# Performance work log

Measured on AMD Instinct MI355X. Metric: run time of the kernel, lower is better.

The kernel has to match this reference:

```python
import jax, jax.numpy as jnp
import numpy as np

B, H, W, DIM = 1, 320, 320, 256
WIN, NH = 10, 8
HD = DIM // NH
N = WIN * WIN
HID = 4 * DIM
SCALE = HD ** (-0.5)
EPS = 1e-5


def _rel_pos_index():
    coords = np.stack(np.meshgrid(np.arange(WIN), np.arange(WIN), indexing='ij'))  # [2,w,w]
    cf = coords.reshape(2, -1)                      # [2, N]
    rel = (cf[:, :, None] - cf[:, None, :]).transpose(1, 2, 0).astype(np.int64)  # [N,N,2]
    rel[:, :, 0] += WIN - 1
    rel[:, :, 1] += WIN - 1
    rel[:, :, 0] *= 2 * WIN - 1
    return jnp.asarray(rel.sum(-1))                 # [N, N]

REL_IDX = _rel_pos_index()


def setup_inputs() -> dict:
    key = jax.random.key(0)
    ks = jax.random.split(key, 16)
    std = 0.02
    return {
        'x': jax.random.normal(ks[0], (B, H * W, DIM), jnp.float32),
        'norm1_g': jnp.ones((DIM,), jnp.float32),
        'norm1_b': jnp.zeros((DIM,), jnp.float32),
        'wq': jax.random.normal(ks[1], (DIM, DIM), jnp.float32) * std,
        'bq': jnp.zeros((DIM,), jnp.float32),
        'wkv': jax.random.normal(ks[2], (DIM, 2 * DIM), jnp.float32) * std,
        'bkv': jnp.zeros((2 * DIM,), jnp.float32),
        'rpb': jax.random.normal(ks[3], ((2 * WIN - 1) ** 2, NH), jnp.float32) * std,
        'proj_w': jax.random.normal(ks[4], (DIM, DIM), jnp.float32) * std,
        'proj_b': jnp.zeros((DIM,), jnp.float32),
        'norm2_g': jnp.ones((DIM,), jnp.float32),
        'norm2_b': jnp.zeros((DIM,), jnp.float32),
        'l1_w': jax.random.normal(ks[5], (DIM, HID), jnp.float32) * std,
        'l1_b': jnp.zeros((HID,), jnp.float32),
        'dw_w': jax.random.normal(ks[6], (HID, 1, 3, 3), jnp.float32) * std,
        'dw_b': jnp.zeros((HID,), jnp.float32),
        'l2_w': jax.random.normal(ks[7], (HID, DIM), jnp.float32) * std,
        'l2_b': jnp.zeros((DIM,), jnp.float32),
    }


def _ln(x, g, b):
    m = x.mean(-1, keepdims=True)
    v = ((x - m) ** 2).mean(-1, keepdims=True)
    return (x - m) * jax.lax.rsqrt(v + EPS) * g + b


def reference(x, norm1_g, norm1_b, wq, bq, wkv, bkv, rpb, proj_w, proj_b,
              norm2_g, norm2_b, l1_w, l1_b, dw_w, dw_b, l2_w, l2_b):
    # ---- Window attention branch ----
    h = _ln(x, norm1_g, norm1_b).reshape(B, H, W, DIM)
    # window partition: [B*nW, N, C]
    win = h.reshape(B, H // WIN, WIN, W // WIN, WIN, DIM)
    win = win.transpose(0, 1, 3, 2, 4, 5).reshape(-1, N, DIM)
    q = (win @ wq + bq).reshape(-1, N, NH, HD).transpose(0, 2, 1, 3) * SCALE  # [bW,h,N,d]
    kv = (win @ wkv + bkv).reshape(-1, N, 2, NH, HD).transpose(2, 0, 3, 1, 4)
    k, v = kv[0], kv[1]                                                        # [bW,h,N,d]
    attn = jnp.einsum('bhnd,bhmd->bhnm', q, k)                                 # [bW,h,N,N]
    bias = rpb[REL_IDX]                                                        # [N,N,h]
    attn = attn + bias.transpose(2, 0, 1)[None]
    attn = jax.nn.softmax(attn, axis=-1)
    o = jnp.einsum('bhnm,bhmd->bhnd', attn, v).transpose(0, 2, 1, 3).reshape(-1, N, DIM)
    o = o @ proj_w + proj_b
    # window reverse: [B, H*W, C]
    o = o.reshape(B, H // WIN, W // WIN, WIN, WIN, DIM)
    o = o.transpose(0, 1, 3, 2, 4, 5).reshape(B, H * W, DIM)
    x = x + o
    # ---- LeFF branch ----
    h2 = _ln(x, norm2_g, norm2_b)
    f = jax.nn.gelu(h2 @ l1_w + l1_b, approximate=False)
    f = f.reshape(B, H, W, HID).transpose(0, 3, 1, 2)                          # NCHW
    f = jax.lax.conv_general_dilated(
        f, dw_w, window_strides=(1, 1), padding='SAME',
        feature_group_count=HID,
        dimension_numbers=('NCHW', 'OIHW', 'NCHW')) + dw_b[None, :, None, None]
    f = jax.nn.gelu(f, approximate=False)
    f = f.transpose(0, 2, 3, 1).reshape(B, H * W, HID)
    x = x + (f @ l2_w + l2_b)
    return x
```

## Files before the change

kernel.cpp:

```cpp
#include <hip/hip_runtime.h>
#include <hip/hip_bf16.h>

typedef unsigned short u16;
typedef __attribute__((ext_vector_type(8))) __bf16 bf16x8;
typedef __attribute__((ext_vector_type(4))) float f32x4;

#define HW_ 320
#define DIM_ 256
#define HID_ 1024
#define SCALE_ 0.1767766952966369f
#define LDP 72
#define NEGINF_ -30000.0f

__device__ __forceinline__ float b2f(u16 u){
  union{unsigned int i; float f;} z; z.i=((unsigned int)u)<<16; return z.f;
}
__device__ __forceinline__ u16 f2b(float f){
  union{float f; unsigned int i;} z; z.f=f;
  return (u16)((z.i + 0x7fffu + ((z.i>>16)&1u))>>16);
}
__device__ __forceinline__ u16 f2b_s(float f, float sub){
  union{float f; unsigned int i;} z; z.f=f;
  if ((z.i & 0x7F800000u) == 0x7F800000u) z.f = sub;
  return (u16)((z.i + 0x7fffu + ((z.i>>16)&1u))>>16);
}
__device__ __forceinline__ float gelu_f(float v){
  float u = 0.7978845608028654f*(v + 0.044715f*v*v*v);
  float e = __expf(2.f*u);
  float t = 1.f - 2.f/(e+1.f);
  return 0.5f*v*(1.f+t);
}

__global__ void k_transpose(const float* __restrict__ src, u16* __restrict__ dst, int K, int N){
  int i = blockIdx.x*256 + threadIdx.x;
  if (i < K*N){ int k = i / N, n = i - k*N; dst[(size_t)n*K + k] = f2b(src[i]); }
}
__global__ void k_transpose_dw(const float* __restrict__ src, u16* __restrict__ dst){
  int i = blockIdx.x*256 + threadIdx.x;
  if (i < 9216){ int ch = i / 9, kk = i - ch*9; dst[kk*1024 + ch] = f2b(src[i]); }
}
__global__ void k_qkvbias(const float* __restrict__ bq, const float* __restrict__ bkv, float* __restrict__ dst){
  int i = blockIdx.x*256 + threadIdx.x;
  if (i < 768) dst[i] = (i<256) ? bq[i] : bkv[i-256];
}
__global__ void k_biastab(const float* __restrict__ rpb, float* __restrict__ btab){
  int i = blockIdx.x*256 + threadIdx.x;
  if (i >= 114688) return;
  int ct = i & 7, lr = (i>>3) & 15;
  int idx = i >> 7;
  int n = idx % 112, h = idx / 112;
  int m = ct*16 + lr;
  float v = NEGINF_;
  if (n < 100 && m < 100){
    int rel = (n/10 - m/10 + 9)*19 + (n%10 - m%10 + 9);
    v = rpb[rel*8 + h];
  }
  btab[i] = v;
}

template<int F32IN, int WINDOWED>
__global__ __launch_bounds__(256) void k_ln(const void* __restrict__ xv,
    const float* __restrict__ g, const float* __restrict__ b, u16* __restrict__ out)
{
  int tid = threadIdx.x, lane = tid & 63;
  int t = blockIdx.x*4 + (tid>>6);
  float v[4];
  if constexpr (F32IN){
    float4 f = *(const float4*)((const float*)xv + (size_t)t*DIM_ + lane*4);
    v[0]=f.x; v[1]=f.y; v[2]=f.z; v[3]=f.w;
  } else {
    uint2 u = *(const uint2*)((const u16*)xv + (size_t)t*DIM_ + lane*4);
    v[0]=b2f((u16)(u.x&0xffff)); v[1]=b2f((u16)(u.x>>16));
    v[2]=b2f((u16)(u.y&0xffff)); v[3]=b2f((u16)(u.y>>16));
  }
  float s  = v[0]+v[1]+v[2]+v[3];
  float ss = v[0]*v[0]+v[1]*v[1]+v[2]*v[2]+v[3]*v[3];
  for (int m=1;m<64;m<<=1){ s += __shfl_xor(s,m,64); ss += __shfl_xor(ss,m,64); }
  float mean = s*(1.0f/DIM_);
  float var  = ss*(1.0f/DIM_) - mean*mean;
  if (var < 0.f) var = 0.f;
  float rstd = rsqrtf(var + 1e-5f);
  float4 gg = *(const float4*)(g + lane*4);
  float4 bb = *(const float4*)(b + lane*4);
  float o0 = (v[0]-mean)*rstd*gg.x + bb.x;
  float o1 = (v[1]-mean)*rstd*gg.y + bb.y;
  float o2 = (v[2]-mean)*rstd*gg.z + bb.z;
  float o3 = (v[3]-mean)*rstd*gg.w + bb.w;
  int row = t;
  if constexpr (WINDOWED){
    int hy = t / HW_, wx = t - hy*HW_;
    row = ((hy/10)*32 + wx/10)*100 + (hy%10)*10 + (wx%10);
  }
  unsigned lo = (unsigned)f2b(o0) | ((unsigned)f2b(o1)<<16);
  unsigned hi = (unsigned)f2b(o2) | ((unsigned)f2b(o3)<<16);
  *(uint2*)(out + (size_t)row*DIM_ + lane*4) = make_uint2(lo,hi);
}

template<int EPI, int CLAMP>
__global__ __launch_bounds__(512,2) void k_gemm(
    const u16* __restrict__ A, const u16* __restrict__ Bt, int K, int nx,
    const float* __restrict__ biasf,
    const float* __restrict__ resf, const u16* __restrict__ resb,
    u16* __restrict__ O0, u16* __restrict__ O1, u16* __restrict__ O2,
    float* __restrict__ Of,
    int a_off, int o_off, int mguard)
{
  __shared__ u16 Al[256*LDP];
  __shared__ u16 Bl[128*LDP];
  int tid = threadIdx.x;
  int bid = blockIdx.x, nwg = gridDim.x;
  int swz = (bid & 7)*(nwg>>3) + (bid>>3);
  int m0 = (swz / nx)*256, n0 = (swz % nx)*128;
  int w = tid>>6, lane = tid&63, lr = lane&15, lg = lane>>4;
  int wrow = (w>>1)*64, wcol = (w&1)*64;
  f32x4 zero = {0.f,0.f,0.f,0.f};
  f32x4 acc[4][4];
  #pragma unroll
  for (int i=0;i<4;++i)
    #pragma unroll
    for (int j=0;j<4;++j) acc[i][j]=zero;

  for (int kt=0; kt<K; kt+=64){
    #pragma unroll
    for (int it=0; it<4; ++it){
      int vi = tid + it*512;
      int row = vi>>3, cv = (vi&7)*8;
      int srow = m0 + row;
      if constexpr (CLAMP){
        srow += a_off;
        srow = srow < 0 ? 0 : (srow > 102399 ? 102399 : srow);
      }
      *(bf16x8*)&Al[row*LDP+cv] = *(const bf16x8*)(A + (size_t)srow*K + kt + cv);
    }
    #pragma unroll
    for (int it=0; it<2; ++it){
      int vi = tid + it*512;
      int row = vi>>3, cv = (vi&7)*8;
      *(bf16x8*)&Bl[row*LDP+cv] = *(const bf16x8*)(Bt + (size_t)(n0+row)*K + kt + cv);
    }
    __syncthreads();
    #pragma unroll
    for (int k0=0;k0<64;k0+=32){
      bf16x8 af[4], bfr[4];
      #pragma unroll
      for (int i=0;i<4;++i) af[i]  = *(const bf16x8*)&Al[(wrow+i*16+lr)*LDP + k0 + lg*8];
      #pragma unroll
      for (int j=0;j<4;++j) bfr[j] = *(const bf16x8*)&Bl[(wcol+j*16+lr)*LDP + k0 + lg*8];
      #pragma unroll
      for (int i=0;i<4;++i)
        #pragma unroll
        for (int j=0;j<4;++j)
          acc[i][j] = __builtin_amdgcn_mfma_f32_16x16x32_bf16(af[i], bfr[j], acc[i][j],0,0,0);
    }
    __syncthreads();
  }

  float bj[4];
  #pragma unroll
  for (int j=0;j<4;++j) bj[j] = biasf[n0 + wcol + j*16 + lr];

  #pragma unroll
  for (int i=0;i<4;++i){
    #pragma unroll
    for (int r=0;r<4;++r){
      int grow = m0 + wrow + i*16 + lg*4 + r;
      if constexpr (EPI==0){
        int winl = grow/100, n = grow - winl*100;
        size_t rowb = ((size_t)winl*8)*3200 + (size_t)n*32;
        #pragma unroll
        for (int j=0;j<4;++j){
          int gcol = n0 + wcol + j*16 + lr;
          float v = acc[i][j][r] + bj[j];
          int part = gcol>>8, c = gcol&255;
          size_t idx = rowb + (size_t)(c>>5)*3200 + (c&31);
          if (part==0)      O0[idx] = f2b_s(v*SCALE_, 10000.f);
          else if (part==1) O1[idx] = f2b_s(v, 10000.f);
          else              O2[idx] = f2b_s(v, 10000.f);
        }
      } else if constexpr (EPI==1){
        int win = grow/100, n = grow - win*100;
        int wy = win>>5, wxx = win&31;
        int py = n/10, px = n - py*10;
        size_t t = (size_t)((wy*10+py)*HW_ + wxx*10 + px);
        #pragma unroll
        for (int j=0;j<4;++j){
          int gcol = n0 + wcol + j*16 + lr;
          float o = acc[i][j][r] + bj[j] + resf[t*DIM_ + gcol];
          O0[t*DIM_ + gcol] = f2b_s(o, 30000.f);
        }
      } else if constexpr (EPI==2){
        if (grow < mguard){
          #pragma unroll
          for (int j=0;j<4;++j){
            int gcol = n0 + wcol + j*16 + lr;
            float o = gelu_f(acc[i][j][r] + bj[j]);
            O0[(size_t)grow*HID_ + gcol] = f2b_s(o, 40000.f);
          }
        }
      } else {
        size_t t = (size_t)(o_off + grow);
        #pragma unroll
        for (int j=0;j<4;++j){
          int gcol = n0 + wcol + j*16 + lr;
          float o = acc[i][j][r] + bj[j] + b2f(resb[t*DIM_ + gcol]);
          union{float f; unsigned int i;} z; z.f=o;
          if ((z.i & 0x7F800000u) == 0x7F800000u) o = 60000.f;
          Of[t*DIM_ + gcol] = o;
        }
      }
    }
  }
}

__global__ __launch_bounds__(256) void k_attn(
    const u16* __restrict__ Q, const u16* __restrict__ Kb, const u16* __restrict__ Vb,
    const float* __restrict__ btab, u16* __restrict__ Ow)
{
  __shared__ u16 p_lds[112*136];
  __shared__ u16 v_t[32*136];
  int tid = threadIdx.x;
  int wh = blockIdx.x;
  int head = wh & 7, win = wh >> 3;
  for (int i=tid;i<896;i+=256){ int row=i>>3, c=i&7; *(unsigned*)&p_lds[row*136 + 112 + 2*c] = 0u; }
  for (int i=tid;i<576;i+=256){ int d=i/18, c=i-18*d; *(unsigned*)&v_t[d*136 + 100 + 2*c] = 0u; }
  __syncthreads();
  const u16* vbase = Vb + (size_t)wh*3200;
  for (int i=tid;i<1600;i+=256){
    int m=i>>4, d2=(i&15)<<1;
    unsigned u = *(const unsigned*)(vbase + m*32 + d2);
    v_t[d2*136+m]     = (u16)(u&0xffff);
    v_t[(d2+1)*136+m] = (u16)(u>>16);
  }

  int w = tid>>6, lane = tid&63, lr = lane&15, lg = lane>>4;
  const u16* qbase = Q  + (size_t)wh*3200;
  const u16* kbase = Kb + (size_t)wh*3200;
  f32x4 zero = {0.f,0.f,0.f,0.f};
  bf16x8 aq[2];
  #pragma unroll
  for (int rt=0;rt<2;++rt){
    int qr = w*32 + rt*16 + lr; if (qr>99) qr=99;
    aq[rt] = *(const bf16x8*)(qbase + qr*32 + lg*8);
  }
  f32x4 s[2][7];
  #pragma unroll
  for (int ct=0;ct<7;++ct){
    int kr = ct*16 + lr; if (kr>99) kr=99;
    bf16x8 bk = *(const bf16x8*)(kbase + kr*32 + lg*8);
    s[0][ct] = __builtin_amdgcn_mfma_f32_16x16x32_bf16(aq[0], bk, zero,0,0,0);
    s[1][ct] = __builtin_amdgcn_mfma_f32_16x16x32_bf16(aq[1], bk, zero,0,0,0);
  }
  float inv[2][4];
  #pragma unroll
  for (int rt=0;rt<2;++rt){
    #pragma unroll
    for (int r=0;r<4;++r){
      int n = w*32 + rt*16 + lg*4 + r;
      int nb = n < 112 ? n : 111;
      const float* brow = btab + (((size_t)(head*112 + nb))*16 + lr)*8;
      float4 b0 = *(const float4*)brow;
      float4 b1 = *(const float4*)(brow + 4);
      float bias7[7] = {b0.x,b0.y,b0.z,b0.w,b1.x,b1.y,b1.z};
      float sm = 0.f;
      #pragma unroll
      for (int ct=0;ct<7;++ct){
        float p = __expf(s[rt][ct][r] + bias7[ct]);
        s[rt][ct][r] = p; sm += p;
      }
      #pragma unroll
      for (int msk=1;msk<16;msk<<=1) sm += __shfl_xor(sm,msk,64);
      inv[rt][r] = 1.f/sm;
      if (n < 112){
        #pragma unroll
        for (int ct=0;ct<7;++ct) p_lds[n*136 + ct*16 + lr] = f2b(s[rt][ct][r]);
      }
    }
  }
  __syncthreads();
  f32x4 o[2][2];
  o[0][0]=zero; o[0][1]=zero; o[1][0]=zero; o[1][1]=zero;
  #pragma unroll
  for (int k0=0;k0<128;k0+=32){
    bf16x8 ap[2];
    #pragma unroll
    for (int rt=0;rt<2;++rt){
      int pr = w*32 + rt*16 + lr; if (pr>111) pr=111;
      ap[rt] = *(const bf16x8*)&p_lds[pr*136 + k0 + lg*8];
    }
    #pragma unroll
    for (int dt=0;dt<2;++dt){
      bf16x8 bv = *(const bf16x8*)&v_t[(dt*16+lr)*136 + k0 + lg*8];
      o[0][dt] = __builtin_amdgcn_mfma_f32_16x16x32_bf16(ap[0], bv, o[0][dt],0,0,0);
      o[1][dt] = __builtin_amdgcn_mfma_f32_16x16x32_bf16(ap[1], bv, o[1][dt],0,0,0);
    }
  }
  #pragma unroll
  for (int rt=0;rt<2;++rt){
    #pragma unroll
    for (int dt=0;dt<2;++dt){
      #pragma unroll
      for (int r=0;r<4;++r){
        int n = w*32 + rt*16 + lg*4 + r;
        if (n<100)
          Ow[((size_t)(win*100+n))*DIM_ + head*32 + dt*16 + lr] = f2b_s(o[rt][dt][r]*inv[rt][r], 20000.f);
      }
    }
  }
}

#define YT_ 10
__global__ __launch_bounds__(256) void k_dwconv2(const u16* __restrict__ f,
    const u16* __restrict__ wT, const float* __restrict__ bias,
    u16* __restrict__ g, int y0)
{
  int tid = threadIdx.x;
  int bid = blockIdx.x;
  int xt = bid % 160, yt = bid / 160;
  int x  = xt*2 + (tid>>7);
  int cg = (tid&127)<<3;
  int yl0 = yt*YT_;

  float w[9][8];
  #pragma unroll
  for (int kk=0;kk<9;++kk){
    uint4 u = *(const uint4*)(wT + kk*1024 + cg);
    const unsigned* up=(const unsigned*)&u;
    #pragma unroll
    for(int e=0;e<4;++e){ w[kk][2*e]=b2f((u16)(up[e]&0xffff)); w[kk][2*e+1]=b2f((u16)(up[e]>>16)); }
  }
  float bs[8];
  {
    float4 b0 = *(const float4*)(bias+cg);
    float4 b1 = *(const float4*)(bias+cg+4);
    bs[0]=b0.x;bs[1]=b0.y;bs[2]=b0.z;bs[3]=b0.w;bs[4]=b1.x;bs[5]=b1.y;bs[6]=b1.z;bs[7]=b1.w;
  }
  uint4 zq = make_uint4(0,0,0,0);
  auto ld = [&](int ytap, int xx)->uint4{
    int yy = y0 + ytap;
    if (xx<0 || xx>=HW_ || yy<0 || yy>=HW_) return zq;
    return *(const uint4*)(f + ((size_t)((ytap+1)*HW_+xx))*HID_ + cg);
  };
  uint4 a00=ld(yl0-1,x-1), a01=ld(yl0-1,x), a02=ld(yl0-1,x+1);
  uint4 a10=ld(yl0  ,x-1), a11=ld(yl0  ,x), a12=ld(yl0  ,x+1);
  #pragma unroll
  for (int r=0;r<YT_;++r){
    int yl = yl0 + r;
    uint4 a20=ld(yl+1,x-1), a21=ld(yl+1,x), a22=ld(yl+1,x+1);
    float acc[8];
    #pragma unroll
    for (int c=0;c<8;++c) acc[c]=bs[c];
    auto fma8 = [&](const uint4& a, const float (&wk)[8]){
      const unsigned* up=(const unsigned*)&a;
      #pragma unroll
      for(int e=0;e<4;++e){
        acc[2*e]   += b2f((u16)(up[e]&0xffff)) * wk[2*e];
        acc[2*e+1] += b2f((u16)(up[e]>>16))    * wk[2*e+1];
      }
    };
    fma8(a00,w[0]); fma8(a01,w[1]); fma8(a02,w[2]);
    fma8(a10,w[3]); fma8(a11,w[4]); fma8(a12,w[5]);
    fma8(a20,w[6]); fma8(a21,w[7]); fma8(a22,w[8]);
    u16 ov[8];
    #pragma unroll
    for (int c=0;c<8;++c) ov[c] = f2b_s(gelu_f(acc[c]), 50000.f);
    uint4 pack;
    pack.x = (unsigned)ov[0] | ((unsigned)ov[1]<<16);
    pack.y = (unsigned)ov[2] | ((unsigned)ov[3]<<16);
    pack.z = (unsigned)ov[4] | ((unsigned)ov[5]<<16);
    pack.w = (unsigned)ov[6] | ((unsigned)ov[7]<<16);
    *(uint4*)(g + ((size_t)(yl*HW_+x))*HID_ + cg) = pack;
    a00=a10;a01=a11;a02=a12; a10=a20;a11=a21;a12=a22;
  }
}

extern "C" void kernel_launch(void* const* d_in, const int* in_sizes, int n_in,
                              void* d_out, int out_size, void* d_ws, size_t ws_size,
                              hipStream_t stream)
{
  (void)in_sizes; (void)n_in; (void)out_size; (void)ws_size;
  const float* x     = (const float*)d_in[0];
  const float* n1g   = (const float*)d_in[1];
  const float* n1b   = (const float*)d_in[2];
  const float* wq    = (const float*)d_in[3];
  const float* bq    = (const float*)d_in[4];
  const float* wkv   = (const float*)d_in[5];
  const float* bkv   = (const float*)d_in[6];
  const float* rpb   = (const float*)d_in[7];
  const float* projw = (const float*)d_in[8];
  const float* projb = (const float*)d_in[9];
  const float* n2g   = (const float*)d_in[10];
  const float* n2b   = (const float*)d_in[11];
  const float* l1w   = (const float*)d_in[12];
  const float* l1b   = (const float*)d_in[13];
  const float* dww   = (const float*)d_in[14];
  const float* dwb   = (const float*)d_in[15];
  const float* l2w   = (const float*)d_in[16];
  const float* l2b   = (const float*)d_in[17];

  char* ws = (char*)d_ws;
  u16*   WqkvT   = (u16*)(ws + 0);
  u16*   projT   = (u16*)(ws + 393216);
  u16*   l1T     = (u16*)(ws + 524288);
  u16*   l2T     = (u16*)(ws + 1048576);
  float* qkvbias = (float*)(ws + 1572864);
  u16*   dwT     = (u16*)(ws + 1575936);
  float* btab    = (float*)(ws + 1594368);
  u16*   x1      = (u16*)(ws + 2097152);
  u16*   h2      = (u16*)(ws + 54525952);
  char*  BR      = ws + 106954752;
  u16* Qb    = (u16*)(BR + 0);
  u16* Kbuf  = (u16*)(BR + 52428800);
  u16* Vbuf  = (u16*)(BR + 104857600);
  u16* hwin  = (u16*)(ws + 264241152);
  u16* fband = (u16*)(BR + 0);
  u16* gband = (u16*)(BR + 106430464);
  u16* owin  = (u16*)d_out;
  float* outp = (float*)d_out;

  k_transpose<<<256, 256, 0, stream>>>(wq,   WqkvT,          256, 256);
  k_transpose<<<512, 256, 0, stream>>>(wkv,  WqkvT + 65536,  256, 512);
  k_transpose<<<256, 256, 0, stream>>>(projw, projT,         256, 256);
  k_transpose<<<1024,256, 0, stream>>>(l1w,  l1T,            256, 1024);
  k_transpose<<<1024,256, 0, stream>>>(l2w,  l2T,            1024, 256);
  k_transpose_dw<<<36, 256, 0, stream>>>(dww, dwT);
  k_qkvbias<<<3, 256, 0, stream>>>(bq, bkv, qkvbias);
  k_biastab<<<448, 256, 0, stream>>>(rpb, btab);

  k_ln<1,1><<<25600, 256, 0, stream>>>(x, n1g, n1b, hwin);
  k_gemm<0,0><<<2400, 512, 0, stream>>>(hwin, WqkvT, 256, 6,
      qkvbias, nullptr, nullptr, Qb, Kbuf, Vbuf, nullptr, 0, 0, 1<<30);
  k_attn<<<8192, 256, 0, stream>>>(Qb, Kbuf, Vbuf, btab, owin);
  k_gemm<1,0><<<800, 512, 0, stream>>>(owin, projT, 256, 2,
      projb, x, nullptr, x1, nullptr, nullptr, nullptr, 0, 0, 1<<30);
  k_ln<0,0><<<25600, 256, 0, stream>>>(x1, n2g, n2b, h2);
  for (int b=0; b<2; ++b){
    int y0 = 160*b;
    k_gemm<2,1><<<1624, 512, 0, stream>>>(h2, l1T, 256, 8,
        l1b, nullptr, nullptr, fband, nullptr, nullptr, nullptr,
        (y0-1)*HW_, 0, 51840);
    k_dwconv2<<<2560, 256, 0, stream>>>(fband, dwT, dwb, gband, y0);
    k_gemm<3,0><<<400, 512, 0, stream>>>(gband, l2T, 1024, 2,
        l2b, nullptr, x1, nullptr, nullptr, nullptr, outp,
        0, y0*HW_, 1<<30);
  }
}
```

Measured before the change: 789.4 us.

## Shrink GEMM tiles, prefetch K-tiles in registers, and store QKV row-major

The GEMM now uses 128x128 tiles with 256 threads instead of 256x128 with 512 threads. It prefetches the next K-tile into registers while the current tile is computed, which removes one barrier per iteration. The QKV GEMM writes a plain row-major [tokens,768] buffer instead of scattering into per-head Q/K/V layouts, and attention reads strided from it. The softmax scale is folded into the Wq weights and bias on the host-side prep kernels. The trade-offs are strided, less coalesced attention loads, more blocks re-reading B tiles, and the removal of the row guard and clamp in epilogues.

```diff
diff --git a/kernel.cpp b/kernel.cpp
--- a/kernel.cpp
+++ b/kernel.cpp
@@ -31,9 +31,10 @@
   return 0.5f*v*(1.f+t);
 }
 
-__global__ void k_transpose(const float* __restrict__ src, u16* __restrict__ dst, int K, int N){
+__global__ void k_transpose(const float* __restrict__ src, u16* __restrict__ dst,
+                            int K, int N, float scale){
   int i = blockIdx.x*256 + threadIdx.x;
-  if (i < K*N){ int k = i / N, n = i - k*N; dst[(size_t)n*K + k] = f2b(src[i]); }
+  if (i < K*N){ int k = i / N, n = i - k*N; dst[(size_t)n*K + k] = f2b(src[i]*scale); }
 }
 __global__ void k_transpose_dw(const float* __restrict__ src, u16* __restrict__ dst){
   int i = blockIdx.x*256 + threadIdx.x;
@@ -41,7 +42,7 @@
 }
 __global__ void k_qkvbias(const float* __restrict__ bq, const float* __restrict__ bkv, float* __restrict__ dst){
   int i = blockIdx.x*256 + threadIdx.x;
-  if (i < 768) dst[i] = (i<256) ? bq[i] : bkv[i-256];
+  if (i < 768) dst[i] = (i<256) ? bq[i]*SCALE_ : bkv[i-256];
 }
 __global__ void k_biastab(const float* __restrict__ rpb, float* __restrict__ btab){
   int i = blockIdx.x*256 + threadIdx.x;
@@ -97,20 +98,19 @@
 }
 
 template<int EPI, int CLAMP>
-__global__ __launch_bounds__(512,2) void k_gemm(
+__global__ __launch_bounds__(256) void k_gemm(
     const u16* __restrict__ A, const u16* __restrict__ Bt, int K, int nx,
     const float* __restrict__ biasf,
     const float* __restrict__ resf, const u16* __restrict__ resb,
-    u16* __restrict__ O0, u16* __restrict__ O1, u16* __restrict__ O2,
-    float* __restrict__ Of,
-    int a_off, int o_off, int mguard)
+    u16* __restrict__ O0, float* __restrict__ Of,
+    int a_off, int o_off)
 {
-  __shared__ u16 Al[256*LDP];
+  __shared__ u16 Al[128*LDP];
   __shared__ u16 Bl[128*LDP];
   int tid = threadIdx.x;
   int bid = blockIdx.x, nwg = gridDim.x;
   int swz = (bid & 7)*(nwg>>3) + (bid>>3);
-  int m0 = (swz / nx)*256, n0 = (swz % nx)*128;
+  int m0 = (swz / nx)*128, n0 = (swz % nx)*128;
   int w = tid>>6, lane = tid&63, lr = lane&15, lg = lane>>4;
   int wrow = (w>>1)*64, wcol = (w&1)*64;
   f32x4 zero = {0.f,0.f,0.f,0.f};
@@ -120,23 +120,36 @@
     #pragma unroll
     for (int j=0;j<4;++j) acc[i][j]=zero;
 
+  const u16* pA[4]; const u16* pB[4];
+  u16* lA[4]; u16* lB[4];
+  #pragma unroll
+  for (int it=0; it<4; ++it){
+    int vi = tid + it*256;
+    int row = vi>>3, cv = (vi&7)*8;
+    int srow = m0 + row;
+    if constexpr (CLAMP){
+      srow += a_off;
+      srow = srow < 0 ? 0 : (srow > 102399 ? 102399 : srow);
+    }
+    pA[it] = A  + (size_t)srow*K + cv;
+    pB[it] = Bt + (size_t)(n0+row)*K + cv;
+    lA[it] = &Al[row*LDP+cv];
+    lB[it] = &Bl[row*LDP+cv];
+  }
+  bf16x8 av[4], bv[4];
+  #pragma unroll
+  for (int it=0; it<4; ++it){ av[it] = *(const bf16x8*)pA[it]; bv[it] = *(const bf16x8*)pB[it]; }
+
   for (int kt=0; kt<K; kt+=64){
-    #pragma unroll
-    for (int it=0; it<4; ++it){
-      int vi = tid + it*512;
-      int row = vi>>3, cv = (vi&7)*8;
-      int srow = m0 + row;
-      if constexpr (CLAMP){
-        srow += a_off;
-        srow = srow < 0 ? 0 : (srow > 102399 ? 102399 : srow);
-      }
-      *(bf16x8*)&Al[row*LDP+cv] = *(const bf16x8*)(A + (size_t)srow*K + kt + cv);
-    }
-    #pragma unroll
-    for (int it=0; it<2; ++it){
-      int vi = tid + it*512;
-      int row = vi>>3, cv = (vi&7)*8;
-      *(bf16x8*)&Bl[row*LDP+cv] = *(const bf16x8*)(Bt + (size_t)(n0+row)*K + kt + cv);
+    __syncthreads();
+    #pragma unroll
+    for (int it=0; it<4; ++it){ *(bf16x8*)lA[it] = av[it]; *(bf16x8*)lB[it] = bv[it]; }
+    if (kt + 64 < K){
+      #pragma unroll
+      for (int it=0; it<4; ++it){
+        av[it] = *(const bf16x8*)(pA[it] + kt + 64);
+        bv[it] = *(const bf16x8*)(pB[it] + kt + 64);
+      }
     }
     __syncthreads();
     #pragma unroll
@@ -152,7 +165,6 @@
         for (int j=0;j<4;++j)
           acc[i][j] = __builtin_amdgcn_mfma_f32_16x16x32_bf16(af[i], bfr[j], acc[i][j],0,0,0);
     }
-    __syncthreads();
   }
 
   float bj[4];
@@ -165,17 +177,11 @@
     for (int r=0;r<4;++r){
       int grow = m0 + wrow + i*16 + lg*4 + r;
       if constexpr (EPI==0){
-        int winl = grow/100, n = grow - winl*100;
-        size_t rowb = ((size_t)winl*8)*3200 + (size_t)n*32;
+        size_t rb = (size_t)grow*768;
         #pragma unroll
         for (int j=0;j<4;++j){
           int gcol = n0 + wcol + j*16 + lr;
-          float v = acc[i][j][r] + bj[j];
-          int part = gcol>>8, c = gcol&255;
-          size_t idx = rowb + (size_t)(c>>5)*3200 + (c&31);
-          if (part==0)      O0[idx] = f2b_s(v*SCALE_, 10000.f);
-          else if (part==1) O1[idx] = f2b_s(v, 10000.f);
-          else              O2[idx] = f2b_s(v, 10000.f);
+          O0[rb + gcol] = f2b_s(acc[i][j][r] + bj[j], 10000.f);
         }
       } else if constexpr (EPI==1){
         int win = grow/100, n = grow - win*100;
@@ -189,13 +195,11 @@
           O0[t*DIM_ + gcol] = f2b_s(o, 30000.f);
         }
       } else if constexpr (EPI==2){
-        if (grow < mguard){
-          #pragma unroll
-          for (int j=0;j<4;++j){
-            int gcol = n0 + wcol + j*16 + lr;
-            float o = gelu_f(acc[i][j][r] + bj[j]);
-            O0[(size_t)grow*HID_ + gcol] = f2b_s(o, 40000.f);
-          }
+        #pragma unroll
+        for (int j=0;j<4;++j){
+          int gcol = n0 + wcol + j*16 + lr;
+          float o = gelu_f(acc[i][j][r] + bj[j]);
+          O0[(size_t)grow*HID_ + gcol] = f2b_s(o, 40000.f);
         }
       } else {
         size_t t = (size_t)(o_off + grow);
@@ -213,8 +217,7 @@
 }
 
 __global__ __launch_bounds__(256) void k_attn(
-    const u16* __restrict__ Q, const u16* __restrict__ Kb, const u16* __restrict__ Vb,
-    const float* __restrict__ btab, u16* __restrict__ Ow)
+    const u16* __restrict__ QKV, const float* __restrict__ btab, u16* __restrict__ Ow)
 {
   __shared__ u16 p_lds[112*136];
   __shared__ u16 v_t[32*136];
@@ -224,29 +227,28 @@
   for (int i=tid;i<896;i+=256){ int row=i>>3, c=i&7; *(unsigned*)&p_lds[row*136 + 112 + 2*c] = 0u; }
   for (int i=tid;i<576;i+=256){ int d=i/18, c=i-18*d; *(unsigned*)&v_t[d*136 + 100 + 2*c] = 0u; }
   __syncthreads();
-  const u16* vbase = Vb + (size_t)wh*3200;
+  const u16* base = QKV + (size_t)(win*100)*768 + head*32;
+  const u16* vbase = base + 512;
   for (int i=tid;i<1600;i+=256){
     int m=i>>4, d2=(i&15)<<1;
-    unsigned u = *(const unsigned*)(vbase + m*32 + d2);
+    unsigned u = *(const unsigned*)(vbase + (size_t)m*768 + d2);
     v_t[d2*136+m]     = (u16)(u&0xffff);
     v_t[(d2+1)*136+m] = (u16)(u>>16);
   }
 
   int w = tid>>6, lane = tid&63, lr = lane&15, lg = lane>>4;
-  const u16* qbase = Q  + (size_t)wh*3200;
-  const u16* kbase = Kb + (size_t)wh*3200;
   f32x4 zero = {0.f,0.f,0.f,0.f};
   bf16x8 aq[2];
   #pragma unroll
   for (int rt=0;rt<2;++rt){
-    int qr = w*32 + rt*16 + lr; if (qr>99) qr=99;
-    aq[rt] = *(const bf16x8*)(qbase + qr*32 + lg*8);
+    int qr = w*32 + rt*16 + lr;
+    aq[rt] = *(const bf16x8*)(base + (size_t)qr*768 + lg*8);
   }
   f32x4 s[2][7];
   #pragma unroll
   for (int ct=0;ct<7;++ct){
-    int kr = ct*16 + lr; if (kr>99) kr=99;
-    bf16x8 bk = *(const bf16x8*)(kbase + kr*32 + lg*8);
+    int kr = ct*16 + lr;
+    bf16x8 bk = *(const bf16x8*)(base + 256 + (size_t)kr*768 + lg*8);
     s[0][ct] = __builtin_amdgcn_mfma_f32_16x16x32_bf16(aq[0], bk, zero,0,0,0);
     s[1][ct] = __builtin_amdgcn_mfma_f32_16x16x32_bf16(aq[1], bk, zero,0,0,0);
   }
@@ -408,39 +410,35 @@
   u16*   x1      = (u16*)(ws + 2097152);
   u16*   h2      = (u16*)(ws + 54525952);
   char*  BR      = ws + 106954752;
-  u16* Qb    = (u16*)(BR + 0);
-  u16* Kbuf  = (u16*)(BR + 52428800);
-  u16* Vbuf  = (u16*)(BR + 104857600);
-  u16* hwin  = (u16*)(ws + 264241152);
+  u16* QKV   = (u16*)(BR + 0);
+  u16* hwin  = (u16*)(ws + 264441856);
   u16* fband = (u16*)(BR + 0);
   u16* gband = (u16*)(BR + 106430464);
   u16* owin  = (u16*)d_out;
   float* outp = (float*)d_out;
 
-  k_transpose<<<256, 256, 0, stream>>>(wq,   WqkvT,          256, 256);
-  k_transpose<<<512, 256, 0, stream>>>(wkv,  WqkvT + 65536,  256, 512);
-  k_transpose<<<256, 256, 0, stream>>>(projw, projT,         256, 256);
-  k_transpose<<<1024,256, 0, stream>>>(l1w,  l1T,            256, 1024);
-  k_transpose<<<1024,256, 0, stream>>>(l2w,  l2T,            1024, 256);
+  k_transpose<<<256, 256, 0, stream>>>(wq,   WqkvT,          256, 256, SCALE_);
+  k_transpose<<<512, 256, 0, stream>>>(wkv,  WqkvT + 65536,  256, 512, 1.f);
+  k_transpose<<<256, 256, 0, stream>>>(projw, projT,         256, 256, 1.f);
+  k_transpose<<<1024,256, 0, stream>>>(l1w,  l1T,            256, 1024, 1.f);
+  k_transpose<<<1024,256, 0, stream>>>(l2w,  l2T,            1024, 256, 1.f);
   k_transpose_dw<<<36, 256, 0, stream>>>(dww, dwT);
   k_qkvbias<<<3, 256, 0, stream>>>(bq, bkv, qkvbias);
   k_biastab<<<448, 256, 0, stream>>>(rpb, btab);
 
   k_ln<1,1><<<25600, 256, 0, stream>>>(x, n1g, n1b, hwin);
-  k_gemm<0,0><<<2400, 512, 0, stream>>>(hwin, WqkvT, 256, 6,
-      qkvbias, nullptr, nullptr, Qb, Kbuf, Vbuf, nullptr, 0, 0, 1<<30);
-  k_attn<<<8192, 256, 0, stream>>>(Qb, Kbuf, Vbuf, btab, owin);
-  k_gemm<1,0><<<800, 512, 0, stream>>>(owin, projT, 256, 2,
-      projb, x, nullptr, x1, nullptr, nullptr, nullptr, 0, 0, 1<<30);
+  k_gemm<0,0><<<4800, 256, 0, stream>>>(hwin, WqkvT, 256, 6,
+      qkvbias, nullptr, nullptr, QKV, nullptr, 0, 0);
+  k_attn<<<8192, 256, 0, stream>>>(QKV, btab, owin);
+  k_gemm<1,0><<<1600, 256, 0, stream>>>(owin, projT, 256, 2,
+      projb, x, nullptr, x1, nullptr, 0, 0);
   k_ln<0,0><<<25600, 256, 0, stream>>>(x1, n2g, n2b, h2);
   for (int b=0; b<2; ++b){
     int y0 = 160*b;
-    k_gemm<2,1><<<1624, 512, 0, stream>>>(h2, l1T, 256, 8,
-        l1b, nullptr, nullptr, fband, nullptr, nullptr, nullptr,
-        (y0-1)*HW_, 0, 51840);
+    k_gemm<2,1><<<3240, 256, 0, stream>>>(h2, l1T, 256, 8,
+        l1b, nullptr, nullptr, fband, nullptr, (y0-1)*HW_, 0);
     k_dwconv2<<<2560, 256, 0, stream>>>(fband, dwT, dwb, gband, y0);
-    k_gemm<3,0><<<400, 512, 0, stream>>>(gband, l2T, 1024, 2,
-        l2b, nullptr, x1, nullptr, nullptr, nullptr, outp,
-        0, y0*HW_, 1<<30);
-  }
-}
+    k_gemm<3,0><<<800, 256, 0, stream>>>(gband, l2T, 1024, 2,
+        l2b, nullptr, x1, nullptr, outp, 0, y0*HW_);
+  }
+}
```

Result: faster. 702.3 us (-11.0%).
